# Kernel optimization log

Hardware: AMD Instinct MI355X
Metric: run time of the kernel (lower is better)

The kernel has to match this reference:

```python
import jax, jax.numpy as jnp
import numpy as np

N_USERS = 200000
N_ENTITY = 1000000
D = 64
B = 16384


def _ragged(rng, avg, lo, hi):
    lens = rng.integers(lo, hi + 1, size=B)
    seg = np.repeat(np.arange(B), lens)
    idx = rng.integers(0, N_ENTITY, size=seg.shape[0])
    return jnp.asarray(idx, jnp.int32), jnp.asarray(seg, jnp.int32)


def setup_inputs() -> dict:
    key = jax.random.key(0)
    ks = jax.random.split(key, 4)
    rng = np.random.default_rng(0)
    a_idx, a_seg = _ragged(rng, 32, 1, 64)   # actors: avg ~32 per movie
    d_idx, d_seg = _ragged(rng, 2, 1, 4)     # directors: avg ~2.5
    g_idx, g_seg = _ragged(rng, 8, 1, 16)    # genres: avg ~8.5
    user_id = jax.random.randint(ks[0], (B,), 0, N_USERS)
    user_factors = jax.random.normal(ks[1], (N_USERS, D), jnp.float32) * 0.1
    entity_factors = jax.random.normal(ks[2], (N_ENTITY, D), jnp.float32) * 0.1
    relation_k = jax.random.normal(ks[3], (D, 3), jnp.float32) * 0.1
    return {
        "user_id": user_id,
        "actors_idx": a_idx, "actors_seg": a_seg,
        "directors_idx": d_idx, "directors_seg": d_seg,
        "genres_idx": g_idx, "genres_seg": g_seg,
        "user_factors": user_factors,
        "entity_factors": entity_factors,
        "relation_k": relation_k,
        "rate": 0,
    }


def _seg_mean_score(idx, seg, users, entity):
    # gather entity rows [E,D], dot with the owning user's vector, mean per group
    dots = jnp.einsum('ed,ed->e', entity[idx], users[seg])
    sums = jax.ops.segment_sum(dots, seg, num_segments=B)
    cnt = jax.ops.segment_sum(jnp.ones_like(dots), seg, num_segments=B)
    return sums / jnp.maximum(cnt, 1.0)


def reference(user_id, actors_idx, actors_seg, directors_idx, directors_seg,
              genres_idx, genres_seg, user_factors, entity_factors, relation_k, rate):
    # eval mode: F.dropout is identity, so `rate` is unused
    users = user_factors[user_id]                                  # [B, D]
    scores = jax.nn.softmax(jax.nn.leaky_relu(users @ relation_k, 0.2), axis=1)  # [B, 3]
    ca = _seg_mean_score(actors_idx, actors_seg, users, entity_factors)
    cd = _seg_mean_score(directors_idx, directors_seg, users, entity_factors)
    cg = _seg_mean_score(genres_idx, genres_seg, users, entity_factors)
    s0, s1, s2 = scores[:, 0], scores[:, 1], scores[:, 2]
    prediction = (ca * s0 + cd * s1 + cg * s2) / (s0 + s1 + s2)
    return (prediction, scores, ca, cd, cg)
```

## Files before the change

### kernel.cpp

```cpp
#include <hip/hip_runtime.h>
#include <hip/hip_bf16.h>

__global__ void prep_kernel(const int* __restrict__ a_seg, int na, int* __restrict__ st_a,
                            const int* __restrict__ d_seg, int nd, int* __restrict__ st_d,
                            const int* __restrict__ g_seg, int ng, int* __restrict__ st_g,
                            const int* __restrict__ user_id,
                            const float* __restrict__ ufac,
                            float* __restrict__ U,
                            int B)
{
    const int ntot = na + nd + ng;
    int t = blockIdx.x * blockDim.x + threadIdx.x;

    if (t < ntot) {
        const int* seg; int* st; int e, n;
        if (t < na)            { seg = a_seg; st = st_a; e = t;            n = na; }
        else if (t < na + nd)  { seg = d_seg; st = st_d; e = t - na;       n = nd; }
        else                   { seg = g_seg; st = st_g; e = t - na - nd;  n = ng; }
        const int s = seg[e];
        if (e == 0 || seg[e - 1] != s) st[s] = e;
        if (e == n - 1) st[B] = n;
        return;
    }
    t -= ntot;
    if (t < B * 16) {
        const int b = t >> 4, lane = t & 15;
        const int uid = user_id[b];
        const float4 v = *reinterpret_cast<const float4*>(ufac + (size_t)uid * 64 + lane * 4);
        *reinterpret_cast<float4*>(U + (size_t)b * 64 + lane * 4) = v;
    }
}

__global__ void dots_kernel(const int* __restrict__ a_idx, const int* __restrict__ a_seg, float* __restrict__ dots_a, int na,
                            const int* __restrict__ d_idx, const int* __restrict__ d_seg, float* __restrict__ dots_d, int nd,
                            const int* __restrict__ g_idx, const int* __restrict__ g_seg, float* __restrict__ dots_g, int ng,
                            const float* __restrict__ U,
                            const float* __restrict__ efac)
{
    const int gid = blockIdx.x * blockDim.x + threadIdx.x;
    const int grp = gid >> 4, lane = gid & 15;
    const int ntot = na + nd + ng;
    const int e0t = 2 * grp;
    if (e0t >= ntot) return;
    const int e1t = e0t + 1;

    auto resolve = [&](int t, const int*& idx, const int*& seg, float*& dots, int& e) {
        if (t < na)           { idx = a_idx; seg = a_seg; dots = dots_a; e = t; }
        else if (t < na + nd) { idx = d_idx; seg = d_seg; dots = dots_d; e = t - na; }
        else                  { idx = g_idx; seg = g_seg; dots = dots_g; e = t - na - nd; }
    };

    const int *idx0, *seg0; float* dp0; int e0;
    resolve(e0t, idx0, seg0, dp0, e0);
    const int s0  = seg0[e0];
    const int ei0 = idx0[e0];

    const bool has1 = (e1t < ntot);
    const int *idx1 = idx0, *seg1 = seg0; float* dp1 = dp0; int e1 = e0;
    if (has1) resolve(e1t, idx1, seg1, dp1, e1);
    const int s1  = has1 ? seg1[e1] : s0;
    const int ei1 = has1 ? idx1[e1] : ei0;

    const float4 ev0 = *reinterpret_cast<const float4*>(efac + (size_t)ei0 * 64 + lane * 4);
    const float4 ev1 = *reinterpret_cast<const float4*>(efac + (size_t)ei1 * 64 + lane * 4);
    const float4 uv0 = *reinterpret_cast<const float4*>(U + (size_t)s0 * 64 + lane * 4);
    const float4 uv1 = *reinterpret_cast<const float4*>(U + (size_t)s1 * 64 + lane * 4);

    float a0 = uv0.x * ev0.x + uv0.y * ev0.y + uv0.z * ev0.z + uv0.w * ev0.w;
    float a1 = uv1.x * ev1.x + uv1.y * ev1.y + uv1.z * ev1.z + uv1.w * ev1.w;

    a0 += __shfl_xor(a0, 1, 64);  a1 += __shfl_xor(a1, 1, 64);
    a0 += __shfl_xor(a0, 2, 64);  a1 += __shfl_xor(a1, 2, 64);
    a0 += __shfl_xor(a0, 4, 64);  a1 += __shfl_xor(a1, 4, 64);
    a0 += __shfl_xor(a0, 8, 64);  a1 += __shfl_xor(a1, 8, 64);

    if (lane == 0) dp0[e0] = a0;
    if (lane == 1 && has1) dp1[e1] = a1;
}

__global__ void final_kernel(const float* __restrict__ dots_a, const int* __restrict__ st_a,
                             const float* __restrict__ dots_d, const int* __restrict__ st_d,
                             const float* __restrict__ dots_g, const int* __restrict__ st_g,
                             const float* __restrict__ U,
                             const float* __restrict__ relk,
                             float* __restrict__ out, int B)
{
    const int gid = blockIdx.x * blockDim.x + threadIdx.x;
    const int b = gid >> 4, lane = gid & 15;
    if (b >= B) return;

    const float4 uv = *reinterpret_cast<const float4*>(U + (size_t)b * 64 + lane * 4);
    const int d0 = lane * 4;
    float s0 = uv.x * relk[(d0 + 0) * 3 + 0] + uv.y * relk[(d0 + 1) * 3 + 0]
             + uv.z * relk[(d0 + 2) * 3 + 0] + uv.w * relk[(d0 + 3) * 3 + 0];
    float s1 = uv.x * relk[(d0 + 0) * 3 + 1] + uv.y * relk[(d0 + 1) * 3 + 1]
             + uv.z * relk[(d0 + 2) * 3 + 1] + uv.w * relk[(d0 + 3) * 3 + 1];
    float s2 = uv.x * relk[(d0 + 0) * 3 + 2] + uv.y * relk[(d0 + 1) * 3 + 2]
             + uv.z * relk[(d0 + 2) * 3 + 2] + uv.w * relk[(d0 + 3) * 3 + 2];

    const int sa = st_a[b], ea = st_a[b + 1];
    const int sd = st_d[b], ed = st_d[b + 1];
    const int sg = st_g[b], eg = st_g[b + 1];
    float ca = 0.f, cd = 0.f, cg = 0.f;
    for (int e = sa + lane; e < ea; e += 16) ca += dots_a[e];
    for (int e = sd + lane; e < ed; e += 16) cd += dots_d[e];
    for (int e = sg + lane; e < eg; e += 16) cg += dots_g[e];

#pragma unroll
    for (int m = 1; m <= 8; m <<= 1) {
        s0 += __shfl_xor(s0, m, 64);
        s1 += __shfl_xor(s1, m, 64);
        s2 += __shfl_xor(s2, m, 64);
        ca += __shfl_xor(ca, m, 64);
        cd += __shfl_xor(cd, m, 64);
        cg += __shfl_xor(cg, m, 64);
    }

    if (lane == 0) {
        ca /= (float)(ea - sa);
        cd /= (float)(ed - sd);
        cg /= (float)(eg - sg);

        s0 = s0 > 0.f ? s0 : 0.2f * s0;
        s1 = s1 > 0.f ? s1 : 0.2f * s1;
        s2 = s2 > 0.f ? s2 : 0.2f * s2;
        const float mx = fmaxf(s0, fmaxf(s1, s2));
        const float x0 = expf(s0 - mx), x1 = expf(s1 - mx), x2 = expf(s2 - mx);
        const float inv = 1.0f / (x0 + x1 + x2);
        const float p0 = x0 * inv, p1 = x1 * inv, p2 = x2 * inv;

        out[b] = (ca * p0 + cd * p1 + cg * p2) / (p0 + p1 + p2);
        out[(size_t)B + 3 * b + 0] = p0;
        out[(size_t)B + 3 * b + 1] = p1;
        out[(size_t)B + 3 * b + 2] = p2;
        out[(size_t)4 * B + b] = ca;
        out[(size_t)5 * B + b] = cd;
        out[(size_t)6 * B + b] = cg;
    }
}

extern "C" void kernel_launch(void* const* d_in, const int* in_sizes, int n_in,
                              void* d_out, int out_size, void* d_ws, size_t ws_size,
                              hipStream_t stream) {
    const int*   user_id = (const int*)  d_in[0];
    const int*   a_idx   = (const int*)  d_in[1];
    const int*   a_seg   = (const int*)  d_in[2];
    const int*   dd_idx  = (const int*)  d_in[3];
    const int*   dd_seg  = (const int*)  d_in[4];
    const int*   g_idx   = (const int*)  d_in[5];
    const int*   g_seg   = (const int*)  d_in[6];
    const float* ufac    = (const float*)d_in[7];
    const float* efac    = (const float*)d_in[8];
    const float* relk    = (const float*)d_in[9];
    float* out = (float*)d_out;

    const int B  = in_sizes[0];
    const int na = in_sizes[1];
    const int nd = in_sizes[3];
    const int ng = in_sizes[5];
    const int ntot = na + nd + ng;

    auto align16 = [](size_t x) { return (x + 15) & ~(size_t)15; };
    char* ws = (char*)d_ws;
    size_t off = 0;
    float* U      = (float*)(ws + off); off += align16((size_t)B * 64 * sizeof(float));
    float* dots_a = (float*)(ws + off); off += align16((size_t)na * sizeof(float));
    float* dots_d = (float*)(ws + off); off += align16((size_t)nd * sizeof(float));
    float* dots_g = (float*)(ws + off); off += align16((size_t)ng * sizeof(float));
    int*   st_a   = (int*)  (ws + off); off += align16((size_t)(B + 1) * sizeof(int));
    int*   st_d   = (int*)  (ws + off); off += align16((size_t)(B + 1) * sizeof(int));
    int*   st_g   = (int*)  (ws + off); off += align16((size_t)(B + 1) * sizeof(int));

    const int threads = 256;

    const int prep_threads = ntot + B * 16;
    prep_kernel<<<(prep_threads + threads - 1) / threads, threads, 0, stream>>>(
        a_seg, na, st_a, dd_seg, nd, st_d, g_seg, ng, st_g, user_id, ufac, U, B);

    const long n_groups = (ntot + 1) / 2;
    const long dots_threads = n_groups * 16;
    dots_kernel<<<(dots_threads + threads - 1) / threads, threads, 0, stream>>>(
        a_idx, a_seg, dots_a, na, dd_idx, dd_seg, dots_d, nd, g_idx, g_seg, dots_g, ng, U, efac);

    const int fin_threads = B * 16;
    final_kernel<<<(fin_threads + threads - 1) / threads, threads, 0, stream>>>(
        dots_a, st_a, dots_d, st_d, dots_g, st_g, U, relk, out, B);
}
```

Baseline: 48.25 us.

## Fuse prep into dots kernel, gather user rows directly, process four entities per group

Removes the separate prep kernel: segment-start detection moves into spare lanes of the dots kernel, and user rows are gathered straight from user_factors through user_id instead of a staged U buffer. Each 16-lane group now handles four entities instead of two, giving more loads in flight per thread. This saves one launch and the U materialization round trip, at the cost of an extra user_id indirection per entity and user rows gathered from a larger table with less locality.

```diff
diff --git a/kernel.cpp b/kernel.cpp
--- a/kernel.cpp
+++ b/kernel.cpp
@@ -1,87 +1,98 @@
 #include <hip/hip_runtime.h>
 #include <hip/hip_bf16.h>
 
-__global__ void prep_kernel(const int* __restrict__ a_seg, int na, int* __restrict__ st_a,
-                            const int* __restrict__ d_seg, int nd, int* __restrict__ st_d,
-                            const int* __restrict__ g_seg, int ng, int* __restrict__ st_g,
+__global__ void dots_kernel(const int* __restrict__ a_idx, const int* __restrict__ a_seg,
+                            float* __restrict__ dots_a, int* __restrict__ st_a, int na,
+                            const int* __restrict__ d_idx, const int* __restrict__ d_seg,
+                            float* __restrict__ dots_d, int* __restrict__ st_d, int nd,
+                            const int* __restrict__ g_idx, const int* __restrict__ g_seg,
+                            float* __restrict__ dots_g, int* __restrict__ st_g, int ng,
                             const int* __restrict__ user_id,
                             const float* __restrict__ ufac,
-                            float* __restrict__ U,
+                            const float* __restrict__ efac,
                             int B)
-{
-    const int ntot = na + nd + ng;
-    int t = blockIdx.x * blockDim.x + threadIdx.x;
-
-    if (t < ntot) {
-        const int* seg; int* st; int e, n;
-        if (t < na)            { seg = a_seg; st = st_a; e = t;            n = na; }
-        else if (t < na + nd)  { seg = d_seg; st = st_d; e = t - na;       n = nd; }
-        else                   { seg = g_seg; st = st_g; e = t - na - nd;  n = ng; }
-        const int s = seg[e];
-        if (e == 0 || seg[e - 1] != s) st[s] = e;
-        if (e == n - 1) st[B] = n;
-        return;
-    }
-    t -= ntot;
-    if (t < B * 16) {
-        const int b = t >> 4, lane = t & 15;
-        const int uid = user_id[b];
-        const float4 v = *reinterpret_cast<const float4*>(ufac + (size_t)uid * 64 + lane * 4);
-        *reinterpret_cast<float4*>(U + (size_t)b * 64 + lane * 4) = v;
-    }
-}
-
-__global__ void dots_kernel(const int* __restrict__ a_idx, const int* __restrict__ a_seg, float* __restrict__ dots_a, int na,
-                            const int* __restrict__ d_idx, const int* __restrict__ d_seg, float* __restrict__ dots_d, int nd,
-                            const int* __restrict__ g_idx, const int* __restrict__ g_seg, float* __restrict__ dots_g, int ng,
-                            const float* __restrict__ U,
-                            const float* __restrict__ efac)
 {
     const int gid = blockIdx.x * blockDim.x + threadIdx.x;
     const int grp = gid >> 4, lane = gid & 15;
     const int ntot = na + nd + ng;
-    const int e0t = 2 * grp;
-    if (e0t >= ntot) return;
-    const int e1t = e0t + 1;
+    const int base = 4 * grp;
+    if (base >= ntot) return;
 
-    auto resolve = [&](int t, const int*& idx, const int*& seg, float*& dots, int& e) {
-        if (t < na)           { idx = a_idx; seg = a_seg; dots = dots_a; e = t; }
-        else if (t < na + nd) { idx = d_idx; seg = d_seg; dots = dots_d; e = t - na; }
-        else                  { idx = g_idx; seg = g_seg; dots = dots_g; e = t - na - nd; }
-    };
+#define RESOLVE(T, IDX, SEG, DP, ST, EL, NN)                                     \
+    if ((T) < na)           { IDX = a_idx; SEG = a_seg; DP = dots_a; ST = st_a; EL = (T);            NN = na; } \
+    else if ((T) < na + nd) { IDX = d_idx; SEG = d_seg; DP = dots_d; ST = st_d; EL = (T) - na;       NN = nd; } \
+    else                    { IDX = g_idx; SEG = g_seg; DP = dots_g; ST = st_g; EL = (T) - na - nd;  NN = ng; }
 
-    const int *idx0, *seg0; float* dp0; int e0;
-    resolve(e0t, idx0, seg0, dp0, e0);
-    const int s0  = seg0[e0];
-    const int ei0 = idx0[e0];
+    const bool v1 = (base + 1 < ntot), v2 = (base + 2 < ntot), v3 = (base + 3 < ntot);
 
-    const bool has1 = (e1t < ntot);
-    const int *idx1 = idx0, *seg1 = seg0; float* dp1 = dp0; int e1 = e0;
-    if (has1) resolve(e1t, idx1, seg1, dp1, e1);
-    const int s1  = has1 ? seg1[e1] : s0;
-    const int ei1 = has1 ? idx1[e1] : ei0;
+    const int *idx0, *seg0; float* dp0; int* st0; int e0, n0;
+    const int *idx1, *seg1; float* dp1; int* st1; int e1, n1;
+    const int *idx2, *seg2; float* dp2; int* st2; int e2, n2;
+    const int *idx3, *seg3; float* dp3; int* st3; int e3, n3;
+    RESOLVE(base, idx0, seg0, dp0, st0, e0, n0);
+    RESOLVE(v1 ? base + 1 : base, idx1, seg1, dp1, st1, e1, n1);
+    RESOLVE(v2 ? base + 2 : base, idx2, seg2, dp2, st2, e2, n2);
+    RESOLVE(v3 ? base + 3 : base, idx3, seg3, dp3, st3, e3, n3);
+#undef RESOLVE
 
-    const float4 ev0 = *reinterpret_cast<const float4*>(efac + (size_t)ei0 * 64 + lane * 4);
-    const float4 ev1 = *reinterpret_cast<const float4*>(efac + (size_t)ei1 * 64 + lane * 4);
-    const float4 uv0 = *reinterpret_cast<const float4*>(U + (size_t)s0 * 64 + lane * 4);
-    const float4 uv1 = *reinterpret_cast<const float4*>(U + (size_t)s1 * 64 + lane * 4);
+    const int s0 = seg0[e0], s1 = seg1[e1], s2 = seg2[e2], s3 = seg3[e3];
+    const int i0 = idx0[e0], i1 = idx1[e1], i2 = idx2[e2], i3 = idx3[e3];
+    const int u0 = user_id[s0], u1 = user_id[s1], u2 = user_id[s2], u3 = user_id[s3];
+
+    const float4 ev0 = *reinterpret_cast<const float4*>(efac + (size_t)i0 * 64 + lane * 4);
+    const float4 ev1 = *reinterpret_cast<const float4*>(efac + (size_t)i1 * 64 + lane * 4);
+    const float4 ev2 = *reinterpret_cast<const float4*>(efac + (size_t)i2 * 64 + lane * 4);
+    const float4 ev3 = *reinterpret_cast<const float4*>(efac + (size_t)i3 * 64 + lane * 4);
+    const float4 uv0 = *reinterpret_cast<const float4*>(ufac + (size_t)u0 * 64 + lane * 4);
+    const float4 uv1 = *reinterpret_cast<const float4*>(ufac + (size_t)u1 * 64 + lane * 4);
+    const float4 uv2 = *reinterpret_cast<const float4*>(ufac + (size_t)u2 * 64 + lane * 4);
+    const float4 uv3 = *reinterpret_cast<const float4*>(ufac + (size_t)u3 * 64 + lane * 4);
 
     float a0 = uv0.x * ev0.x + uv0.y * ev0.y + uv0.z * ev0.z + uv0.w * ev0.w;
     float a1 = uv1.x * ev1.x + uv1.y * ev1.y + uv1.z * ev1.z + uv1.w * ev1.w;
+    float a2 = uv2.x * ev2.x + uv2.y * ev2.y + uv2.z * ev2.z + uv2.w * ev2.w;
+    float a3 = uv3.x * ev3.x + uv3.y * ev3.y + uv3.z * ev3.z + uv3.w * ev3.w;
 
-    a0 += __shfl_xor(a0, 1, 64);  a1 += __shfl_xor(a1, 1, 64);
-    a0 += __shfl_xor(a0, 2, 64);  a1 += __shfl_xor(a1, 2, 64);
-    a0 += __shfl_xor(a0, 4, 64);  a1 += __shfl_xor(a1, 4, 64);
-    a0 += __shfl_xor(a0, 8, 64);  a1 += __shfl_xor(a1, 8, 64);
+#pragma unroll
+    for (int m = 1; m <= 8; m <<= 1) {
+        a0 += __shfl_xor(a0, m, 64);
+        a1 += __shfl_xor(a1, m, 64);
+        a2 += __shfl_xor(a2, m, 64);
+        a3 += __shfl_xor(a3, m, 64);
+    }
 
-    if (lane == 0) dp0[e0] = a0;
-    if (lane == 1 && has1) dp1[e1] = a1;
+    if (lane == 0)       dp0[e0] = a0;
+    if (lane == 1 && v1) dp1[e1] = a1;
+    if (lane == 2 && v2) dp2[e2] = a2;
+    if (lane == 3 && v3) dp3[e3] = a3;
+
+    if (lane == 4) {
+        const int prev = (e0 > 0) ? seg0[e0 - 1] : -1;
+        if (prev != s0) st0[s0] = e0;
+        if (e0 == n0 - 1) st0[B] = n0;
+    }
+    if (lane == 5 && v1) {
+        const int prev = (e1 > 0) ? seg1[e1 - 1] : -1;
+        if (prev != s1) st1[s1] = e1;
+        if (e1 == n1 - 1) st1[B] = n1;
+    }
+    if (lane == 6 && v2) {
+        const int prev = (e2 > 0) ? seg2[e2 - 1] : -1;
+        if (prev != s2) st2[s2] = e2;
+        if (e2 == n2 - 1) st2[B] = n2;
+    }
+    if (lane == 7 && v3) {
+        const int prev = (e3 > 0) ? seg3[e3 - 1] : -1;
+        if (prev != s3) st3[s3] = e3;
+        if (e3 == n3 - 1) st3[B] = n3;
+    }
 }
 
 __global__ void final_kernel(const float* __restrict__ dots_a, const int* __restrict__ st_a,
                              const float* __restrict__ dots_d, const int* __restrict__ st_d,
                              const float* __restrict__ dots_g, const int* __restrict__ st_g,
-                             const float* __restrict__ U,
+                             const int* __restrict__ user_id,
+                             const float* __restrict__ ufac,
                              const float* __restrict__ relk,
                              float* __restrict__ out, int B)
 {
@@ -89,7 +100,8 @@
     const int b = gid >> 4, lane = gid & 15;
     if (b >= B) return;
 
-    const float4 uv = *reinterpret_cast<const float4*>(U + (size_t)b * 64 + lane * 4);
+    const int uid = user_id[b];
+    const float4 uv = *reinterpret_cast<const float4*>(ufac + (size_t)uid * 64 + lane * 4);
     const int d0 = lane * 4;
     float s0 = uv.x * relk[(d0 + 0) * 3 + 0] + uv.y * relk[(d0 + 1) * 3 + 0]
              + uv.z * relk[(d0 + 2) * 3 + 0] + uv.w * relk[(d0 + 3) * 3 + 0];
@@ -163,7 +175,6 @@
     auto align16 = [](size_t x) { return (x + 15) & ~(size_t)15; };
     char* ws = (char*)d_ws;
     size_t off = 0;
-    float* U      = (float*)(ws + off); off += align16((size_t)B * 64 * sizeof(float));
     float* dots_a = (float*)(ws + off); off += align16((size_t)na * sizeof(float));
     float* dots_d = (float*)(ws + off); off += align16((size_t)nd * sizeof(float));
     float* dots_g = (float*)(ws + off); off += align16((size_t)ng * sizeof(float));
@@ -173,16 +184,15 @@
 
     const int threads = 256;
 
-    const int prep_threads = ntot + B * 16;
-    prep_kernel<<<(prep_threads + threads - 1) / threads, threads, 0, stream>>>(
-        a_seg, na, st_a, dd_seg, nd, st_d, g_seg, ng, st_g, user_id, ufac, U, B);
-
-    const long n_groups = (ntot + 1) / 2;
+    const long n_groups = (ntot + 3) / 4;
     const long dots_threads = n_groups * 16;
     dots_kernel<<<(dots_threads + threads - 1) / threads, threads, 0, stream>>>(
-        a_idx, a_seg, dots_a, na, dd_idx, dd_seg, dots_d, nd, g_idx, g_seg, dots_g, ng, U, efac);
+        a_idx, a_seg, dots_a, st_a, na,
+        dd_idx, dd_seg, dots_d, st_d, nd,
+        g_idx, g_seg, dots_g, st_g, ng,
+        user_id, ufac, efac, B);
 
     const int fin_threads = B * 16;
     final_kernel<<<(fin_threads + threads - 1) / threads, threads, 0, stream>>>(
-        dots_a, st_a, dots_d, st_d, dots_g, st_g, U, relk, out, B);
+        dots_a, st_a, dots_d, st_d, dots_g, st_g, user_id, ufac, relk, out, B);
 }
```

Result: faster. 46.98 us, median of 2 (-2.6%).
